# Kernel tuning notes

Hardware: AMD Instinct MI355X
Metric: run time of the kernel (lower is better)

Reference implementation:

```python
import jax, jax.numpy as jnp
import numpy as np
import math

NEG_INF = -1e38


def wkv_scan(w, u, k, v):
    """Numerically-stable RWKV WKV recurrence.
    w, u: [C] (w is already -exp(time_decay)); k, v: [B, T, C] -> y: [B, T, C]."""
    B, T, C = k.shape

    def step(carry, kv_t):
        a, b, pp = carry            # running num/den in log-max form, [B, C]
        kt, vt = kv_t               # [B, C]
        ww = u + kt
        q = jnp.maximum(pp, ww)
        e1 = jnp.exp(pp - q)
        e2 = jnp.exp(ww - q)
        y = (e1 * a + e2 * vt) / (e1 * b + e2)
        # state update with decay w
        ww2 = pp + w
        q2 = jnp.maximum(ww2, kt)
        e1b = jnp.exp(ww2 - q2)
        e2b = jnp.exp(kt - q2)
        return (e1b * a + e2b * vt, e1b * b + e2b, q2), y

    init = (jnp.zeros((B, C), k.dtype), jnp.zeros((B, C), k.dtype),
            jnp.full((B, C), NEG_INF, k.dtype))
    kT = jnp.swapaxes(k, 0, 1)      # [T, B, C]
    vT = jnp.swapaxes(v, 0, 1)
    _, ys = jax.lax.scan(step, init, (kT, vT))
    return jnp.swapaxes(ys, 0, 1)   # [B, T, C]


def setup_inputs() -> dict:
    key = jax.random.key(0)
    B, T, C = 16, 1024, 1024
    k1, k2, k3, k4 = jax.random.split(key, 4)
    x = jax.random.normal(k1, (B, T, C), dtype=jnp.float32)
    scale = 0.02
    Wk = jax.random.normal(k2, (C, C), dtype=jnp.float32) * scale
    Wr = jax.random.normal(k3, (C, C), dtype=jnp.float32) * scale
    Wo = jax.random.normal(k4, (C, C), dtype=jnp.float32) * scale
    # faithful parameter init from RWKVTimeMix.__init__
    h = np.arange(C, dtype=np.float64)
    decay_speed = -5.0 + 8.0 * (h / (C - 1)) ** (0.7 + 1.3 * 1)
    zigzag = (((np.arange(C) + 1) % 3) - 1) * 0.5
    time_first = np.ones(C) * math.log(0.3) + zigzag
    return {
        "x": x,
        "Wk": Wk,
        "Wr": Wr,
        "Wo": Wo,
        "time_decay": jnp.asarray(decay_speed, dtype=jnp.float32),
        "time_first": jnp.asarray(time_first, dtype=jnp.float32),
    }


def reference(x, Wk, Wr, Wo, time_decay, time_first):
    # k = key(x); r = receptance(x); NOTE: source uses receptance for v as well
    k = jnp.einsum('btc,hc->bth', x, Wk)
    r = jnp.einsum('btc,hc->bth', x, Wr)
    v = r  # faithful to source: v = self.receptance(input)
    w = -jnp.exp(time_decay)
    y = wkv_scan(w, time_first, k, v)
    out = jax.nn.sigmoid(r) * y
    return jnp.einsum('bth,ch->btc', out, Wo)
```

## Files before the change

kernel.cpp:

```cpp
#include <hip/hip_runtime.h>
#include <hip/hip_bf16.h>


typedef __attribute__((ext_vector_type(8))) short bf16x8;
typedef __attribute__((ext_vector_type(4))) float f32x4;
typedef unsigned short u16;

#define GK   1024
#define NKT  16
#define ROWB 2048l

__device__ __forceinline__ void async_copy16(const void* g, void* l) {
    __builtin_amdgcn_global_load_lds(
        (const __attribute__((address_space(1))) void*)g,
        (__attribute__((address_space(3))) void*)l,
        16 , 0 , 0 );
}

__global__ __launch_bounds__(256) void cast_f32_bf16_kernel(
    const float* __restrict__ src, __hip_bfloat16* __restrict__ dst, int n)
{
    const int i = (blockIdx.x * 256 + threadIdx.x) * 4;
    if (i + 3 < n) {
        const f32x4 v = *(const f32x4*)(src + i);
        __hip_bfloat16 o[4];
        o[0] = __float2bfloat16(v[0]);
        o[1] = __float2bfloat16(v[1]);
        o[2] = __float2bfloat16(v[2]);
        o[3] = __float2bfloat16(v[3]);
        *(__attribute__((ext_vector_type(4))) short*)(dst + i) =
            *(__attribute__((ext_vector_type(4))) short*)o;
    }
}


#define PHASE(I0, STAGE_STMT) do {                                            \
    bf16x8 a00 = *(const bf16x8*)(As + arow + (I0) * 2048 + ck0);             \
    bf16x8 a01 = *(const bf16x8*)(As + arow + (I0) * 2048 + ck1);             \
    bf16x8 a10 = *(const bf16x8*)(As + arow + (I0 + 1) * 2048 + ck0);         \
    bf16x8 a11 = *(const bf16x8*)(As + arow + (I0 + 1) * 2048 + ck1);         \
    STAGE_STMT;                                                               \
    __builtin_amdgcn_s_barrier();                                             \
    asm volatile("s_waitcnt lgkmcnt(0)" ::: "memory");                        \
    __builtin_amdgcn_sched_barrier(0);                                        \
    __builtin_amdgcn_s_setprio(1);                                            \
    _Pragma("unroll")                                                         \
    for (int n = 0; n < 4; ++n) {                                             \
        acc[I0][n]     = __builtin_amdgcn_mfma_f32_16x16x32_bf16(             \
                             a00, bf[n][0], acc[I0][n], 0, 0, 0);             \
        acc[I0][n]     = __builtin_amdgcn_mfma_f32_16x16x32_bf16(             \
                             a01, bf[n][1], acc[I0][n], 0, 0, 0);             \
        acc[I0 + 1][n] = __builtin_amdgcn_mfma_f32_16x16x32_bf16(             \
                             a10, bf[n][0], acc[I0 + 1][n], 0, 0, 0);         \
        acc[I0 + 1][n] = __builtin_amdgcn_mfma_f32_16x16x32_bf16(             \
                             a11, bf[n][1], acc[I0 + 1][n], 0, 0, 0);         \
    }                                                                         \
    __builtin_amdgcn_s_setprio(0);                                            \
    __builtin_amdgcn_s_barrier();                                             \
} while (0)

template <typename OutT>
__global__ __launch_bounds__(512, 2) void gemm256_kernel(
    const __hip_bfloat16* __restrict__ A,
    const __hip_bfloat16* __restrict__ B0,
    const __hip_bfloat16* __restrict__ B1,
    OutT* __restrict__ C,
    int ldc, int nsplit, int ntn)
{
    __shared__ __align__(16) char lds[131072];

    const int tid = threadIdx.x;

    const int nwg = gridDim.x;
    const int cpx = nwg >> 3;
    const int wg  = blockIdx.x;
    const int swz = (wg & 7) * cpx + (wg >> 3);
    const int bm  = (swz / ntn) * 256;
    const int bn  = (swz % ntn) * 256;

    const __hip_bfloat16* Bsrc;
    int bnl;
    if (bn < nsplit) { Bsrc = B0; bnl = bn; }
    else             { Bsrc = B1; bnl = bn - nsplit; }

    const int lane = tid & 63;
    const int wave = tid >> 6;
    const int nl   = lane & 15;
    const int quad = lane >> 4;
    const int wm   = (wave >> 2) * 128;
    const int wn   = (wave & 3) * 64;

    const int r0 = tid >> 3;
    const int cs = ((tid & 7) ^ (r0 & 7)) << 4;
    const int od = tid * 16;
    const char* Ag = (const char*)A    + (size_t)(bm  + r0) * ROWB + cs;
    const char* Bg = (const char*)Bsrc + (size_t)(bnl + r0) * ROWB + cs;

    char* ldsA0 = lds;
    char* ldsB0 = lds + 32768;
    char* ldsA1 = lds + 65536;
    char* ldsB1 = lds + 98304;

    auto stageA = [&](int kt, int h, char* dstA) {
        const char* g = Ag + (size_t)h * 128 * ROWB + (size_t)kt * 128;
        async_copy16(g,             dstA + h * 16384 + od);
        async_copy16(g + 64 * ROWB, dstA + h * 16384 + od + 8192);
    };
    auto stageB = [&](int kt, int h, char* dstB) {
        const char* g = Bg + (size_t)h * 128 * ROWB + (size_t)kt * 128;
        async_copy16(g,             dstB + h * 16384 + od);
        async_copy16(g + 64 * ROWB, dstB + h * 16384 + od + 8192);
    };

    const int rw   = nl & 7;
    const int ck0  = (quad ^ rw) << 4;
    const int ck1  = ((4 + quad) ^ rw) << 4;
    const int arow = (wm + nl) * 128;
    const int brow = (wn + nl) * 128;

    f32x4 acc[8][4] = {};

    stageB(0, 0, ldsB0); stageB(0, 1, ldsB0);
    stageA(0, 0, ldsA0); stageA(0, 1, ldsA0);
    stageB(1, 0, ldsB1); stageB(1, 1, ldsB1);
    asm volatile("s_waitcnt vmcnt(4)" ::: "memory");
    __builtin_amdgcn_s_barrier();

#pragma unroll 2
    for (int t = 0; t < NKT; ++t) {
        char* As = (t & 1) ? ldsA1 : ldsA0;
        char* Bs = (t & 1) ? ldsB1 : ldsB0;
        char* Ao = (t & 1) ? ldsA0 : ldsA1;

        bf16x8 bf[4][2];
#pragma unroll
        for (int n = 0; n < 4; ++n) {
            bf[n][0] = *(const bf16x8*)(Bs + brow + n * 2048 + ck0);
            bf[n][1] = *(const bf16x8*)(Bs + brow + n * 2048 + ck1);
        }

        PHASE(0, if (t + 1 < NKT) stageA(t + 1, 0, Ao));
        PHASE(2, if (t + 1 < NKT) stageA(t + 1, 1, Ao));
        PHASE(4, if (t + 2 < NKT) stageB(t + 2, 0, Bs));
        PHASE(6, {
            if (t + 2 < NKT) {
                stageB(t + 2, 1, Bs);
                asm volatile("s_waitcnt vmcnt(4)" ::: "memory");
            } else {
                asm volatile("s_waitcnt vmcnt(0)" ::: "memory");
            }
        });
    }

#pragma unroll
    for (int i = 0; i < 8; ++i) {
#pragma unroll
        for (int n = 0; n < 4; ++n) {
            const int col = bn + wn + n * 16 + nl;
#pragma unroll
            for (int r = 0; r < 4; ++r) {
                const int m = bm + wm + i * 16 + quad * 4 + r;
                const float vv = acc[i][n][r];
                if constexpr (__is_same(OutT, float))
                    C[(size_t)m * ldc + col] = vv;
                else
                    C[(size_t)m * ldc + col] = __float2bfloat16(vv);
            }
        }
    }
}

#define L2E 1.4426950408889634f

struct Blk { u16 k[8]; u16 v[8]; };

__device__ __forceinline__ void load8(const u16* kp, const u16* vp,
                                      int t, int S, Blk& B) {
#pragma unroll
    for (int j = 0; j < 8; ++j) {
        B.k[j] = kp[(size_t)(t + j) * S];
        B.v[j] = vp[(size_t)(t + j) * S];
    }
}

__device__ __forceinline__ float bf2f(u16 r) {
    return __uint_as_float(((unsigned)r) << 16);
}

__device__ __forceinline__ void wkv_step(
    u16 kraw, u16 vraw, float u2, float w2,
    float& a, float& bb, float& pp2, __hip_bfloat16* op)
{
    const float kf = bf2f(kraw);
    const float vf = bf2f(vraw);
    const float k2 = kf * L2E;

    const float ww2 = u2 + k2;
    const float s   = __builtin_amdgcn_exp2f(fminf(pp2 - ww2, 60.f));
    const float num = s * a + vf;
    const float den = s * bb + 1.f;
    const float e   = __builtin_amdgcn_exp2f(-L2E * vf);
    const float res = num * __builtin_amdgcn_rcpf(den * (1.f + e));
    *op = __float2bfloat16(res);

    const float d   = pp2 + w2 - k2;
    const float m0  = fminf(d, 0.f);
    const float e1b = __builtin_amdgcn_exp2f(m0);
    const float e2b = __builtin_amdgcn_exp2f(m0 - d);
    a   = e1b * a  + e2b * vf;
    bb  = e1b * bb + e2b;
    pp2 = k2 + fmaxf(d, 0.f);
}

__global__ __launch_bounds__(64) void wkv_scan_kernel(
    const __hip_bfloat16* __restrict__ kr,
    const float* __restrict__ tf,
    const float* __restrict__ td,
    __hip_bfloat16* __restrict__ sy,
    int T, int C)
{
    const int gid = blockIdx.x * 64 + threadIdx.x;
    const int b = gid / C;
    const int c = gid - b * C;
    const int S = 2 * C;

    const float u2 = tf[c] * L2E;
    const float w2 = -__expf(td[c]) * L2E;

    float a = 0.f, bb = 0.f, pp2 = -1.4427e38f;

    const u16* kp = (const u16*)(kr + (size_t)b * T * S + c);
    const u16* vp = kp + C;
    __hip_bfloat16* op = sy + (size_t)b * T * C + c;

    Blk A, Bq;
    load8(kp, vp, 0, S, A);

    for (int tb = 0; tb < T; tb += 16) {
        load8(kp, vp, tb + 8, S, Bq);
#pragma unroll
        for (int j = 0; j < 8; ++j)
            wkv_step(A.k[j], A.v[j], u2, w2, a, bb, pp2,
                     op + (size_t)(tb + j) * C);
        if (tb + 16 < T) load8(kp, vp, tb + 16, S, A);
#pragma unroll
        for (int j = 0; j < 8; ++j)
            wkv_step(Bq.k[j], Bq.v[j], u2, w2, a, bb, pp2,
                     op + (size_t)(tb + 8 + j) * C);
    }
}

extern "C" void kernel_launch(void* const* d_in, const int* in_sizes, int n_in,
                              void* d_out, int out_size, void* d_ws, size_t ws_size,
                              hipStream_t stream) {
    const float* x  = (const float*)d_in[0];
    const float* Wk = (const float*)d_in[1];
    const float* Wr = (const float*)d_in[2];
    const float* Wo = (const float*)d_in[3];
    const float* td = (const float*)d_in[4];
    const float* tf = (const float*)d_in[5];
    float* out = (float*)d_out;

    const int B = 16, T = 1024, C = 1024;
    const int M = B * T;
    const int MC = M * C;
    const int CC = C * C;

    __hip_bfloat16* xb  = (__hip_bfloat16*)d_ws;
    __hip_bfloat16* Wkb = xb + (size_t)MC;
    __hip_bfloat16* Wrb = Wkb + (size_t)CC;
    __hip_bfloat16* Wob = Wrb + (size_t)CC;
    __hip_bfloat16* sy  = xb;

    __hip_bfloat16* kr = (__hip_bfloat16*)d_out;

    cast_f32_bf16_kernel<<<MC / 1024, 256, 0, stream>>>(x,  xb,  MC);
    cast_f32_bf16_kernel<<<CC / 1024, 256, 0, stream>>>(Wk, Wkb, CC);
    cast_f32_bf16_kernel<<<CC / 1024, 256, 0, stream>>>(Wr, Wrb, CC);
    cast_f32_bf16_kernel<<<CC / 1024, 256, 0, stream>>>(Wo, Wob, CC);

    gemm256_kernel<__hip_bfloat16><<<dim3((M / 256) * (2 * C / 256)), 512, 0,
                                     stream>>>(xb, Wkb, Wrb, kr, 2 * C, C, 8);

    wkv_scan_kernel<<<dim3((B * C) / 64), 64, 0, stream>>>(
        kr, tf, td, sy, T, C);

    gemm256_kernel<float><<<dim3((M / 256) * (C / 256)), 512, 0, stream>>>(
        sy, Wob, Wob, out, C, C, 4);
}
```

Measured before the change: 311.6 us.

## Split WKV recurrence into chunked two-pass parallel scan

Replaces the sequential per-channel WKV scan over all T steps with a two-pass chunked scan. The first pass computes each 64-step chunk's state aggregate, and the second pass combines the earlier chunk aggregates with decay before emitting outputs for its own chunk. This raises thread-level parallelism from B*C threads to B*C*16, addressing low occupancy and the latency of the serial scan. In exchange it reads k/v twice, adds an O(chunk) prefix-combine loop per thread, and reuses the freed bf16 weight buffers in the workspace as float aggregate storage.

```diff
diff --git a/kernel.cpp b/kernel.cpp
--- a/kernel.cpp
+++ b/kernel.cpp
@@ -9,6 +9,10 @@
 #define GK   1024
 #define NKT  16
 #define ROWB 2048l
+
+#define NCH  16384
+#define NC   16
+#define CL   64
 
 __device__ __forceinline__ void async_copy16(const void* g, void* l) {
     __builtin_amdgcn_global_load_lds(
@@ -56,7 +60,7 @@
                              a11, bf[n][1], acc[I0 + 1][n], 0, 0, 0);         \
     }                                                                         \
     __builtin_amdgcn_s_setprio(0);                                            \
-    __builtin_amdgcn_s_barrier();                                             \
+    __builtin_amdgcn_s_barrier();                                            \
 } while (0)
 
 template <typename OutT>
@@ -187,6 +191,21 @@
     return __uint_as_float(((unsigned)r) << 16);
 }
 
+__device__ __forceinline__ void wkv_state_step(
+    u16 kraw, u16 vraw, float w2, float& a, float& bb, float& pp2)
+{
+    const float kf = bf2f(kraw);
+    const float vf = bf2f(vraw);
+    const float k2 = kf * L2E;
+    const float d   = pp2 + w2 - k2;
+    const float m0  = fminf(d, 0.f);
+    const float e1b = __builtin_amdgcn_exp2f(m0);
+    const float e2b = __builtin_amdgcn_exp2f(m0 - d);
+    a   = e1b * a  + e2b * vf;
+    bb  = e1b * bb + e2b;
+    pp2 = k2 + fmaxf(d, 0.f);
+}
+
 __device__ __forceinline__ void wkv_step(
     u16 kraw, u16 vraw, float u2, float w2,
     float& a, float& bb, float& pp2, __hip_bfloat16* op)
@@ -212,37 +231,89 @@
     pp2 = k2 + fmaxf(d, 0.f);
 }
 
-__global__ __launch_bounds__(64) void wkv_scan_kernel(
+__global__ __launch_bounds__(256) void wkv_agg_kernel(
     const __hip_bfloat16* __restrict__ kr,
-    const float* __restrict__ tf,
     const float* __restrict__ td,
-    __hip_bfloat16* __restrict__ sy,
-    int T, int C)
-{
-    const int gid = blockIdx.x * 64 + threadIdx.x;
-    const int b = gid / C;
-    const int c = gid - b * C;
+    float* __restrict__ aggA, float* __restrict__ aggB,
+    float* __restrict__ aggP, int T, int C)
+{
+    const int gid2  = blockIdx.x * 256 + threadIdx.x;
+    const int ch    = gid2 & (NCH - 1);
+    const int chunk = gid2 >> 14;
+    const int b = ch >> 10;
+    const int c = ch & (C - 1);
+    const int S = 2 * C;
+
+    const float w2 = -__expf(td[c]) * L2E;
+
+    const u16* kp = (const u16*)(kr + (size_t)b * T * S + c)
+                    + (size_t)(chunk * CL) * S;
+    const u16* vp = kp + C;
+
+    float a = 0.f, bb = 0.f, pp2 = -1.4427e38f;
+
+    Blk A, Bq;
+    load8(kp, vp, 0, S, A);
+    for (int tb = 0; tb < CL; tb += 16) {
+        load8(kp, vp, tb + 8, S, Bq);
+#pragma unroll
+        for (int j = 0; j < 8; ++j)
+            wkv_state_step(A.k[j], A.v[j], w2, a, bb, pp2);
+        if (tb + 16 < CL) load8(kp, vp, tb + 16, S, A);
+#pragma unroll
+        for (int j = 0; j < 8; ++j)
+            wkv_state_step(Bq.k[j], Bq.v[j], w2, a, bb, pp2);
+    }
+    aggA[gid2] = a;
+    aggB[gid2] = bb;
+    aggP[gid2] = pp2;
+}
+
+__global__ __launch_bounds__(256) void wkv_out_kernel(
+    const __hip_bfloat16* __restrict__ kr,
+    const float* __restrict__ tf, const float* __restrict__ td,
+    const float* __restrict__ aggA, const float* __restrict__ aggB,
+    const float* __restrict__ aggP,
+    __hip_bfloat16* __restrict__ sy, int T, int C)
+{
+    const int gid2  = blockIdx.x * 256 + threadIdx.x;
+    const int ch    = gid2 & (NCH - 1);
+    const int chunk = gid2 >> 14;
+    const int b = ch >> 10;
+    const int c = ch & (C - 1);
     const int S = 2 * C;
 
     const float u2 = tf[c] * L2E;
     const float w2 = -__expf(td[c]) * L2E;
 
     float a = 0.f, bb = 0.f, pp2 = -1.4427e38f;
-
-    const u16* kp = (const u16*)(kr + (size_t)b * T * S + c);
+    for (int j = 0; j < chunk; ++j) {
+        const float p  = aggP[j * NCH + ch]
+                         + (float)((chunk - 1 - j) * CL) * w2;
+        const float Aj = aggA[j * NCH + ch];
+        const float Bj = aggB[j * NCH + ch];
+        const float q  = fmaxf(pp2, p);
+        const float e1 = __builtin_amdgcn_exp2f(pp2 - q);
+        const float e2 = __builtin_amdgcn_exp2f(p - q);
+        a   = e1 * a  + e2 * Aj;
+        bb  = e1 * bb + e2 * Bj;
+        pp2 = q;
+    }
+
+    const int t0 = chunk * CL;
+    const u16* kp = (const u16*)(kr + (size_t)b * T * S + c) + (size_t)t0 * S;
     const u16* vp = kp + C;
-    __hip_bfloat16* op = sy + (size_t)b * T * C + c;
+    __hip_bfloat16* op = sy + (size_t)b * T * C + (size_t)t0 * C + c;
 
     Blk A, Bq;
     load8(kp, vp, 0, S, A);
-
-    for (int tb = 0; tb < T; tb += 16) {
+    for (int tb = 0; tb < CL; tb += 16) {
         load8(kp, vp, tb + 8, S, Bq);
 #pragma unroll
         for (int j = 0; j < 8; ++j)
             wkv_step(A.k[j], A.v[j], u2, w2, a, bb, pp2,
                      op + (size_t)(tb + j) * C);
-        if (tb + 16 < T) load8(kp, vp, tb + 16, S, A);
+        if (tb + 16 < CL) load8(kp, vp, tb + 16, S, A);
 #pragma unroll
         for (int j = 0; j < 8; ++j)
             wkv_step(Bq.k[j], Bq.v[j], u2, w2, a, bb, pp2,
@@ -272,6 +343,10 @@
     __hip_bfloat16* Wob = Wrb + (size_t)CC;
     __hip_bfloat16* sy  = xb;
 
+    float* aggA = (float*)Wkb;
+    float* aggB = aggA + (size_t)NCH * NC;
+    float* aggP = (float*)Wrb;
+
     __hip_bfloat16* kr = (__hip_bfloat16*)d_out;
 
     cast_f32_bf16_kernel<<<MC / 1024, 256, 0, stream>>>(x,  xb,  MC);
@@ -282,8 +357,11 @@
     gemm256_kernel<__hip_bfloat16><<<dim3((M / 256) * (2 * C / 256)), 512, 0,
                                      stream>>>(xb, Wkb, Wrb, kr, 2 * C, C, 8);
 
-    wkv_scan_kernel<<<dim3((B * C) / 64), 64, 0, stream>>>(
-        kr, tf, td, sy, T, C);
+    wkv_agg_kernel<<<dim3(NCH * NC / 256), 256, 0, stream>>>(
+        kr, td, aggA, aggB, aggP, T, C);
+
+    wkv_out_kernel<<<dim3(NCH * NC / 256), 256, 0, stream>>>(
+        kr, tf, td, aggA, aggB, aggP, sy, T, C);
 
     gemm256_kernel<float><<<dim3((M / 256) * (C / 256)), 512, 0, stream>>>(
         sy, Wob, Wob, out, C, C, 4);
```

Result: faster. 264.1 us (-15.2%).

## Parallelize WKV scan over time chunks and merge cast kernels

Applied to the files above, without the earlier changes.

The sequential WKV scan is replaced by a chunked parallel scan. Each of 16 waves per block scans 64 timesteps to compute local state, publishes it through LDS, combines the preceding chunks' states with decay, then re-runs its chunk to emit outputs. This exposes 16x more parallelism than one thread per channel walking all 1024 steps, at the cost of a second pass of exp work and 64 registers per thread holding k/v. The four f32-to-bf16 cast launches are also merged into a single kernel.

```diff
diff --git a/kernel.cpp b/kernel.cpp
--- a/kernel.cpp
+++ b/kernel.cpp
@@ -4,11 +4,17 @@
 
 typedef __attribute__((ext_vector_type(8))) short bf16x8;
 typedef __attribute__((ext_vector_type(4))) float f32x4;
+typedef __attribute__((ext_vector_type(4))) short s16x4;
 typedef unsigned short u16;
+typedef unsigned int u32;
 
 #define GK   1024
 #define NKT  16
 #define ROWB 2048l
+
+#define NCH  16384
+#define SNC  16
+#define SCL  64
 
 __device__ __forceinline__ void async_copy16(const void* g, void* l) {
     __builtin_amdgcn_global_load_lds(
@@ -17,20 +23,29 @@
         16 , 0 , 0 );
 }
 
-__global__ __launch_bounds__(256) void cast_f32_bf16_kernel(
-    const float* __restrict__ src, __hip_bfloat16* __restrict__ dst, int n)
-{
-    const int i = (blockIdx.x * 256 + threadIdx.x) * 4;
-    if (i + 3 < n) {
-        const f32x4 v = *(const f32x4*)(src + i);
-        __hip_bfloat16 o[4];
-        o[0] = __float2bfloat16(v[0]);
-        o[1] = __float2bfloat16(v[1]);
-        o[2] = __float2bfloat16(v[2]);
-        o[3] = __float2bfloat16(v[3]);
-        *(__attribute__((ext_vector_type(4))) short*)(dst + i) =
-            *(__attribute__((ext_vector_type(4))) short*)o;
-    }
+__global__ __launch_bounds__(256) void cast_all_kernel(
+    const float* __restrict__ x,  const float* __restrict__ wk,
+    const float* __restrict__ wr, const float* __restrict__ wo,
+    __hip_bfloat16* __restrict__ xb,  __hip_bfloat16* __restrict__ wkb,
+    __hip_bfloat16* __restrict__ wrb, __hip_bfloat16* __restrict__ wob)
+{
+    const int bid = blockIdx.x;
+    const float* src;
+    __hip_bfloat16* dst;
+    int blk;
+    if (bid < 16384)      { src = x;  dst = xb;  blk = bid; }
+    else if (bid < 17408) { src = wk; dst = wkb; blk = bid - 16384; }
+    else if (bid < 18432) { src = wr; dst = wrb; blk = bid - 17408; }
+    else                  { src = wo; dst = wob; blk = bid - 18432; }
+
+    const int i = blk * 1024 + threadIdx.x * 4;
+    const f32x4 v = *(const f32x4*)(src + i);
+    __hip_bfloat16 o[4];
+    o[0] = __float2bfloat16(v[0]);
+    o[1] = __float2bfloat16(v[1]);
+    o[2] = __float2bfloat16(v[2]);
+    o[3] = __float2bfloat16(v[3]);
+    *(s16x4*)(dst + i) = *(s16x4*)o;
 }
 
 
@@ -56,7 +71,7 @@
                              a11, bf[n][1], acc[I0 + 1][n], 0, 0, 0);         \
     }                                                                         \
     __builtin_amdgcn_s_setprio(0);                                            \
-    __builtin_amdgcn_s_barrier();                                             \
+    __builtin_amdgcn_s_barrier();                                            \
 } while (0)
 
 template <typename OutT>
@@ -172,19 +187,23 @@
 
 #define L2E 1.4426950408889634f
 
-struct Blk { u16 k[8]; u16 v[8]; };
-
-__device__ __forceinline__ void load8(const u16* kp, const u16* vp,
-                                      int t, int S, Blk& B) {
-#pragma unroll
-    for (int j = 0; j < 8; ++j) {
-        B.k[j] = kp[(size_t)(t + j) * S];
-        B.v[j] = vp[(size_t)(t + j) * S];
-    }
-}
-
 __device__ __forceinline__ float bf2f(u16 r) {
-    return __uint_as_float(((unsigned)r) << 16);
+    return __uint_as_float(((u32)r) << 16);
+}
+
+__device__ __forceinline__ void wkv_state_step(
+    u16 kraw, u16 vraw, float w2, float& a, float& bb, float& pp2)
+{
+    const float kf = bf2f(kraw);
+    const float vf = bf2f(vraw);
+    const float k2 = kf * L2E;
+    const float d   = pp2 + w2 - k2;
+    const float m0  = fminf(d, 0.f);
+    const float e1b = __builtin_amdgcn_exp2f(m0);
+    const float e2b = __builtin_amdgcn_exp2f(m0 - d);
+    a   = e1b * a  + e2b * vf;
+    bb  = e1b * bb + e2b;
+    pp2 = k2 + fmaxf(d, 0.f);
 }
 
 __device__ __forceinline__ void wkv_step(
@@ -212,42 +231,60 @@
     pp2 = k2 + fmaxf(d, 0.f);
 }
 
-__global__ __launch_bounds__(64) void wkv_scan_kernel(
+__global__ __launch_bounds__(1024, 4) void wkv_fused_kernel(
     const __hip_bfloat16* __restrict__ kr,
-    const float* __restrict__ tf,
-    const float* __restrict__ td,
+    const float* __restrict__ tf, const float* __restrict__ td,
     __hip_bfloat16* __restrict__ sy,
     int T, int C)
 {
-    const int gid = blockIdx.x * 64 + threadIdx.x;
-    const int b = gid / C;
-    const int c = gid - b * C;
-    const int S = 2 * C;
+    __shared__ float aggA[SNC][64], aggB[SNC][64], aggP[SNC][64];
+
+    const int tid = threadIdx.x;
+    const int cl  = tid & 63;
+    const int q   = tid >> 6;
+    const int ch  = blockIdx.x * 64 + cl;
+    const int b   = ch >> 10;
+    const int c   = ch & (C - 1);
+    const int S   = 2 * C;
 
     const float u2 = tf[c] * L2E;
     const float w2 = -__expf(td[c]) * L2E;
 
+    const u16* kp = (const u16*)kr + ((size_t)b * T + q * SCL) * S + c;
+    const u16* vp = kp + C;
+
+    u32 kv[SCL];
     float a = 0.f, bb = 0.f, pp2 = -1.4427e38f;
-
-    const u16* kp = (const u16*)(kr + (size_t)b * T * S + c);
-    const u16* vp = kp + C;
-    __hip_bfloat16* op = sy + (size_t)b * T * C + c;
-
-    Blk A, Bq;
-    load8(kp, vp, 0, S, A);
-
-    for (int tb = 0; tb < T; tb += 16) {
-        load8(kp, vp, tb + 8, S, Bq);
-#pragma unroll
-        for (int j = 0; j < 8; ++j)
-            wkv_step(A.k[j], A.v[j], u2, w2, a, bb, pp2,
-                     op + (size_t)(tb + j) * C);
-        if (tb + 16 < T) load8(kp, vp, tb + 16, S, A);
-#pragma unroll
-        for (int j = 0; j < 8; ++j)
-            wkv_step(Bq.k[j], Bq.v[j], u2, w2, a, bb, pp2,
-                     op + (size_t)(tb + 8 + j) * C);
+#pragma unroll
+    for (int t = 0; t < SCL; ++t) {
+        const u16 kraw = kp[(size_t)t * S];
+        const u16 vraw = vp[(size_t)t * S];
+        kv[t] = (u32)kraw | ((u32)vraw << 16);
+        wkv_state_step(kraw, vraw, w2, a, bb, pp2);
     }
+    aggA[q][cl] = a;
+    aggB[q][cl] = bb;
+    aggP[q][cl] = pp2;
+    __syncthreads();
+
+    a = 0.f; bb = 0.f; pp2 = -1.4427e38f;
+    for (int j = 0; j < q; ++j) {
+        const float p  = aggP[j][cl] + (float)((q - 1 - j) * SCL) * w2;
+        const float Aj = aggA[j][cl];
+        const float Bj = aggB[j][cl];
+        const float qm = fmaxf(pp2, p);
+        const float e1 = __builtin_amdgcn_exp2f(pp2 - qm);
+        const float e2 = __builtin_amdgcn_exp2f(p - qm);
+        a   = e1 * a  + e2 * Aj;
+        bb  = e1 * bb + e2 * Bj;
+        pp2 = qm;
+    }
+
+    __hip_bfloat16* op = sy + ((size_t)b * T + q * SCL) * C + c;
+#pragma unroll
+    for (int t = 0; t < SCL; ++t)
+        wkv_step((u16)(kv[t] & 0xffff), (u16)(kv[t] >> 16), u2, w2,
+                 a, bb, pp2, op + (size_t)t * C);
 }
 
 extern "C" void kernel_launch(void* const* d_in, const int* in_sizes, int n_in,
@@ -274,15 +311,13 @@
 
     __hip_bfloat16* kr = (__hip_bfloat16*)d_out;
 
-    cast_f32_bf16_kernel<<<MC / 1024, 256, 0, stream>>>(x,  xb,  MC);
-    cast_f32_bf16_kernel<<<CC / 1024, 256, 0, stream>>>(Wk, Wkb, CC);
-    cast_f32_bf16_kernel<<<CC / 1024, 256, 0, stream>>>(Wr, Wrb, CC);
-    cast_f32_bf16_kernel<<<CC / 1024, 256, 0, stream>>>(Wo, Wob, CC);
+    cast_all_kernel<<<dim3(16384 + 3 * 1024), 256, 0, stream>>>(
+        x, Wk, Wr, Wo, xb, Wkb, Wrb, Wob);
 
     gemm256_kernel<__hip_bfloat16><<<dim3((M / 256) * (2 * C / 256)), 512, 0,
                                      stream>>>(xb, Wkb, Wrb, kr, 2 * C, C, 8);
 
-    wkv_scan_kernel<<<dim3((B * C) / 64), 64, 0, stream>>>(
+    wkv_fused_kernel<<<dim3(NCH / 64), 1024, 0, stream>>>(
         kr, tf, td, sy, T, C);
 
     gemm256_kernel<float><<<dim3((M / 256) * (C / 256)), 512, 0, stream>>>(
```

Measured after the change: 554.9 us. +78.1%, slower.
